# Kernel optimization log

Measured on AMD Instinct MI355X. Metric: run time of the kernel, lower is better.

Reference implementation:

```python
import jax, jax.numpy as jnp
import numpy as np

H = 16          # num_heads
EPS = 1e-6      # RMSNorm eps


def setup_inputs() -> dict:
    key = jax.random.key(0)
    ks = jax.random.split(key, 5)
    B, N, D = 4, 4096, 1024
    x = jax.random.normal(ks[0], (B, N, D), dtype=jnp.float32)
    q = jax.random.normal(ks[1], (D,), dtype=jnp.float32)
    k = jax.random.normal(ks[2], (D,), dtype=jnp.float32)
    log_decay = jax.random.normal(ks[3], (H,), dtype=jnp.float32)
    norm_weight = jnp.ones((D,), dtype=jnp.float32)
    o_w = jax.random.normal(ks[4], (D, D), dtype=jnp.float32) * 0.02
    return {"x": x, "q": q, "k": k, "log_decay": log_decay,
            "norm_weight": norm_weight, "o_w": o_w}


def reference(x, q, k, log_decay, norm_weight, o_w):
    b, n, dm = x.shape
    dh = dm // H
    qh = q.reshape(H, dh)            # per-head query vector (constant over b, n)
    kh = k.reshape(H, dh)            # per-head key vector
    v = x.reshape(b, n, H, dh)       # values = input tokens
    # exp(logsigmoid(a)) == sigmoid(a): per-head decay in (0, 1)
    lam = jax.nn.sigmoid(log_decay)  # (H,)

    def step(S, v_t):
        # S: (b, H, dh, dh) recurrent state;  v_t: (b, H, dh)
        S = lam[None, :, None, None] * S + kh[None, :, :, None] * v_t[:, :, None, :]
        o_t = jnp.einsum('hd,bhdv->bhv', qh, S)
        return S, o_t

    S0 = jnp.zeros((b, H, dh, dh), dtype=x.dtype)
    _, o = jax.lax.scan(step, S0, jnp.moveaxis(v, 1, 0))  # o: (n, b, H, dh)
    o = jnp.moveaxis(o, 0, 1).reshape(b, n, dm)

    # RMSNorm over the channel dim
    o = o * jax.lax.rsqrt(jnp.mean(o * o, axis=-1, keepdims=True) + EPS) * norm_weight
    # o_proj (no bias)
    return o @ o_w.T
```

## Files before the change

### kernel.cpp

```cpp
#include <hip/hip_runtime.h>
#include <hip/hip_bf16.h>
#include <cstdint>
#include <cstddef>

#define HH   16
#define BB   4
#define NN   4096
#define DD   1024
#define MM   (BB * NN)
#define NC   128
#define LC   32
#define EPSV 1e-6f

typedef short short8 __attribute__((ext_vector_type(8)));
typedef float floatx4 __attribute__((ext_vector_type(4)));

__device__ __forceinline__ void async_copy16(const void* g, void* l) {
    __builtin_amdgcn_global_load_lds(
        (const __attribute__((address_space(1))) void*)g,
        (__attribute__((address_space(3))) void*)l, 16, 0, 0);
}

__device__ __forceinline__ uint2 pack_bf16x4(float a, float b, float c, float d) {
    union { __hip_bfloat16 h[4]; uint2 u; } cv;
    cv.h[0] = __float2bfloat16(a); cv.h[1] = __float2bfloat16(b);
    cv.h[2] = __float2bfloat16(c); cv.h[3] = __float2bfloat16(d);
    return cv.u;
}

__global__ void k_meta(const float* __restrict__ q, const float* __restrict__ k,
                       const float* __restrict__ ld, float* __restrict__ meta) {
    int tid = threadIdx.x;
    float p = q[tid] * k[tid];
    #pragma unroll
    for (int off = 32; off > 0; off >>= 1) p += __shfl_xor(p, off);
    if ((tid & 63) == 0) meta[16 + (tid >> 6)] = p;
    if (tid < HH) meta[tid] = 1.f / (1.f + expf(-ld[tid]));
}

__global__ void k_wconv(const float* __restrict__ ow, const float* __restrict__ nw,
                        __hip_bfloat16* __restrict__ wp) {
    size_t i4 = (size_t)blockIdx.x * 256 + threadIdx.x;
    int j = (int)((i4 * 4) & (DD - 1));
    float4 v = ((const float4*)ow)[i4];
    ((uint2*)wp)[i4] = pack_bf16x4(v.x * nw[j], v.y * nw[j + 1],
                                   v.z * nw[j + 2], v.w * nw[j + 3]);
}

__global__ void k_chunk_end(const float* __restrict__ x, const float* __restrict__ meta,
                            float* __restrict__ E) {
    int b = blockIdx.x >> 7, c = blockIdx.x & (NC - 1);
    int j4 = threadIdx.x;
    float lam = meta[(j4 * 4) >> 6];
    const float4* xp = (const float4*)(x + ((size_t)(b * NN + c * LC)) * DD) + j4;
    float4 e = {0.f, 0.f, 0.f, 0.f};
    #pragma unroll
    for (int t = 0; t < LC; ++t) {
        float4 v = xp[(size_t)t * (DD / 4)];
        e.x = fmaf(lam, e.x, v.x); e.y = fmaf(lam, e.y, v.y);
        e.z = fmaf(lam, e.z, v.z); e.w = fmaf(lam, e.w, v.w);
    }
    ((float4*)(E + (size_t)blockIdx.x * DD))[j4] = e;
}

__global__ void k_carry(const float* __restrict__ meta, const float* __restrict__ E,
                        float* __restrict__ P) {
    __shared__ float tile[NC][33];
    int b = blockIdx.x >> 5, jg = blockIdx.x & 31;
    int tid = threadIdx.x;
    int cc = tid >> 5, jj = tid & 31;
    #pragma unroll
    for (int it = 0; it < 16; ++it) {
        int c = it * 8 + cc;
        tile[c][jj] = E[(size_t)(b * NC + c) * DD + jg * 32 + jj];
    }
    __syncthreads();
    if (tid < 32) {
        int j = jg * 32 + tid;
        float lam = meta[j >> 6];
        float lamL = lam;
        lamL *= lamL; lamL *= lamL; lamL *= lamL; lamL *= lamL; lamL *= lamL;
        float p = 0.f;
        for (int c = 0; c < NC; ++c) {
            float e = tile[c][tid];
            tile[c][tid] = p;
            p = fmaf(lamL, p, e);
        }
    }
    __syncthreads();
    #pragma unroll
    for (int it = 0; it < 16; ++it) {
        int c = it * 8 + cc;
        P[(size_t)(b * NC + c) * DD + jg * 32 + jj] = tile[c][jj];
    }
}

__global__ void k_scan(const float* __restrict__ x, const float* __restrict__ meta,
                       const float* __restrict__ P, __hip_bfloat16* __restrict__ obf,
                       float* __restrict__ sumsq) {
    __shared__ float ssq[4][LC];
    int b = blockIdx.x >> 7, c = blockIdx.x & (NC - 1);
    int j4 = threadIdx.x;
    int h = (j4 * 4) >> 6;
    float lam = meta[h];
    float ch  = meta[16 + h];
    int row0 = b * NN + c * LC;
    int lane = threadIdx.x & 63, w = threadIdx.x >> 6;
    const float4* xp = (const float4*)(x + (size_t)row0 * DD) + j4;
    float4 y = ((const float4*)(P + (size_t)blockIdx.x * DD))[j4];
    for (int t = 0; t < LC; ++t) {
        float4 v = xp[(size_t)t * (DD / 4)];
        y.x = fmaf(lam, y.x, v.x); y.y = fmaf(lam, y.y, v.y);
        y.z = fmaf(lam, y.z, v.z); y.w = fmaf(lam, y.w, v.w);
        float ox = ch * y.x, oy = ch * y.y, oz = ch * y.z, ow = ch * y.w;
        ((uint2*)(obf + (size_t)(row0 + t) * DD))[j4] = pack_bf16x4(ox, oy, oz, ow);
        float s = ox * ox + oy * oy + oz * oz + ow * ow;
        #pragma unroll
        for (int off = 32; off > 0; off >>= 1) s += __shfl_xor(s, off);
        if (lane == 0) ssq[w][t] = s;
    }
    __syncthreads();
    if (threadIdx.x < LC) {
        int t = threadIdx.x;
        sumsq[row0 + t] = ssq[0][t] + ssq[1][t] + ssq[2][t] + ssq[3][t];
    }
}

#define GEMM_STAGE(BUF, MAT, KK, TN)                                           \
  do {                                                                         \
    const short* _src = (MAT) ? Wg : Ag;                                       \
    const int _b0 = (MAT) ? n0 : m0;                                           \
    char* _dst = (char*)&lds[BUF][MAT][KK][0] + w * 1024;                      \
    _Pragma("unroll") for (int _i = 0; _i < 2; ++_i)                           \
      async_copy16(_src + (size_t)(_b0 + _i * 128 + rr) * 1024                 \
                        + (TN) * 64 + (KK) * 32 + oo * 8,                      \
                   _dst + _i * 8192);                                          \
  } while (0)

#define GEMM_REGION(BUF, KK)                                                   \
  do {                                                                         \
    short8 af[8]; short8 bf[4];                                                \
    _Pragma("unroll") for (int mt = 0; mt < 8; ++mt)                           \
      af[mt] = *(const short8*)(&lds[BUF][0][KK][0] +                          \
                                (arow_base + mt * 16) * 32 + p_rd * 8);        \
    _Pragma("unroll") for (int nt = 0; nt < 4; ++nt)                           \
      bf[nt] = *(const short8*)(&lds[BUF][1][KK][0] +                          \
                                (brow_base + nt * 16) * 32 + p_rd * 8);        \
    __builtin_amdgcn_s_setprio(1);                                             \
    _Pragma("unroll") for (int mt = 0; mt < 8; ++mt) {                         \
      _Pragma("unroll") for (int nt = 0; nt < 4; ++nt)                         \
        acc[mt][nt] = __builtin_amdgcn_mfma_f32_16x16x32_bf16(                 \
            af[mt], bf[nt], acc[mt][nt], 0, 0, 0);                             \
    }                                                                          \
    __builtin_amdgcn_s_setprio(0);                                             \
  } while (0)

__launch_bounds__(512, 2)
__global__ void k_gemm(const __hip_bfloat16* __restrict__ A,
                       const __hip_bfloat16* __restrict__ W,
                       const float* __restrict__ sumsq, float* __restrict__ out) {
    __shared__ __attribute__((aligned(16))) short lds[2][2][2][256 * 32];
    const int tid = threadIdx.x;
    const int lane = tid & 63, w = tid >> 6;
    const int wm = w >> 2, wn = w & 3;
    const int g = blockIdx.x;
    const int xcd = g & 7, idx = g >> 3;
    const int bm = xcd * 8 + (idx >> 2);
    const int bn = idx & 3;
    const int m0 = bm * 256, n0 = bn * 256;
    const short* Ag = (const short*)A;
    const short* Wg = (const short*)W;

    const int rr = tid >> 2;
    const int oo = (tid & 3) ^ ((rr >> 1) & 3);

    const int p_rd = (lane >> 4) ^ (((lane & 15) >> 1) & 3);
    const int arow_base = wm * 128 + (lane & 15);
    const int brow_base = wn * 64 + (lane & 15);

    floatx4 acc[8][4] = {};

    GEMM_STAGE(0, 0, 0, 0); GEMM_STAGE(0, 1, 0, 0);
    GEMM_STAGE(0, 0, 1, 0); GEMM_STAGE(0, 1, 1, 0);

    for (int t = 0; t < 16; ++t) {
        const int buf = t & 1;
        asm volatile("s_waitcnt vmcnt(4)" ::: "memory");
        __builtin_amdgcn_s_barrier();
        if (t < 15) { GEMM_STAGE(buf ^ 1, 0, 0, t + 1); GEMM_STAGE(buf ^ 1, 1, 0, t + 1); }
        GEMM_REGION(buf, 0);
        if (t < 15) {
            asm volatile("s_waitcnt vmcnt(4)" ::: "memory");
        } else {
            asm volatile("s_waitcnt vmcnt(0)" ::: "memory");
        }
        __builtin_amdgcn_s_barrier();
        if (t < 15) { GEMM_STAGE(buf ^ 1, 0, 1, t + 1); GEMM_STAGE(buf ^ 1, 1, 1, t + 1); }
        GEMM_REGION(buf, 1);
    }

    #pragma unroll
    for (int mt = 0; mt < 8; ++mt) {
        #pragma unroll
        for (int r = 0; r < 4; ++r) {
            int mrow = m0 + wm * 128 + mt * 16 + (lane >> 4) * 4 + r;
            float rs = rsqrtf(sumsq[mrow] * (1.f / 1024.f) + EPSV);
            #pragma unroll
            for (int nt = 0; nt < 4; ++nt) {
                int col = n0 + wn * 64 + nt * 16 + (lane & 15);
                out[(size_t)mrow * 1024 + col] = acc[mt][nt][r] * rs;
            }
        }
    }
}

extern "C" void kernel_launch(void* const* d_in, const int* in_sizes, int n_in,
                              void* d_out, int out_size, void* d_ws, size_t ws_size,
                              hipStream_t stream) {
    const float* x  = (const float*)d_in[0];
    const float* q  = (const float*)d_in[1];
    const float* k  = (const float*)d_in[2];
    const float* ld = (const float*)d_in[3];
    const float* nw = (const float*)d_in[4];
    const float* ow = (const float*)d_in[5];
    float* out = (float*)d_out;

    char* ws = (char*)d_ws;
    float* meta  = (float*)(ws + 0);
    float* sumsq = (float*)(ws + 256);
    float* E     = (float*)(ws + 65792);
    float* P     = (float*)(ws + 2162944);
    __hip_bfloat16* Wp  = (__hip_bfloat16*)(ws + 4260096);
    __hip_bfloat16* Obf = (__hip_bfloat16*)(ws + 6357248);

    k_meta<<<1, 1024, 0, stream>>>(q, k, ld, meta);
    k_wconv<<<(DD * DD / 4) / 256, 256, 0, stream>>>(ow, nw, Wp);
    k_chunk_end<<<BB * NC, 256, 0, stream>>>(x, meta, E);
    k_carry<<<BB * 32, 256, 0, stream>>>(meta, E, P);
    k_scan<<<BB * NC, 256, 0, stream>>>(x, meta, P, Obf, sumsq);
    k_gemm<<<(MM / 256) * (DD / 256), 512, 0, stream>>>(Obf, Wp, sumsq, out);
}
```

Before: 176.3 us.

## Inline meta computation into consumers and deepen GEMM pipeline to 4-stage ring

Removes the k_meta launch by computing sigmoid decay and the per-head q·k dot product inside the scan kernels (with a 16-lane shuffle reduction in k_scan). The GEMM main loop moves from double-buffered halves of a 64-wide K tile to a 4-slot ring of 32-wide K slices, with three slices prefetched ahead and one barrier per slice. The aim is to cut a kernel launch and hide more global-load latency in the GEMM. The cost is more barriers per K and some redundant sigmoid/dot work per block.

```diff
diff --git a/kernel.cpp b/kernel.cpp
--- a/kernel.cpp
+++ b/kernel.cpp
@@ -28,14 +28,8 @@
     return cv.u;
 }
 
-__global__ void k_meta(const float* __restrict__ q, const float* __restrict__ k,
-                       const float* __restrict__ ld, float* __restrict__ meta) {
-    int tid = threadIdx.x;
-    float p = q[tid] * k[tid];
-    #pragma unroll
-    for (int off = 32; off > 0; off >>= 1) p += __shfl_xor(p, off);
-    if ((tid & 63) == 0) meta[16 + (tid >> 6)] = p;
-    if (tid < HH) meta[tid] = 1.f / (1.f + expf(-ld[tid]));
+__device__ __forceinline__ float sigmoidf(float a) {
+    return 1.f / (1.f + expf(-a));
 }
 
 __global__ void k_wconv(const float* __restrict__ ow, const float* __restrict__ nw,
@@ -47,11 +41,11 @@
                                    v.z * nw[j + 2], v.w * nw[j + 3]);
 }
 
-__global__ void k_chunk_end(const float* __restrict__ x, const float* __restrict__ meta,
+__global__ void k_chunk_end(const float* __restrict__ x, const float* __restrict__ ld,
                             float* __restrict__ E) {
     int b = blockIdx.x >> 7, c = blockIdx.x & (NC - 1);
     int j4 = threadIdx.x;
-    float lam = meta[(j4 * 4) >> 6];
+    float lam = sigmoidf(ld[j4 >> 4]);
     const float4* xp = (const float4*)(x + ((size_t)(b * NN + c * LC)) * DD) + j4;
     float4 e = {0.f, 0.f, 0.f, 0.f};
     #pragma unroll
@@ -63,7 +57,7 @@
     ((float4*)(E + (size_t)blockIdx.x * DD))[j4] = e;
 }
 
-__global__ void k_carry(const float* __restrict__ meta, const float* __restrict__ E,
+__global__ void k_carry(const float* __restrict__ ld, const float* __restrict__ E,
                         float* __restrict__ P) {
     __shared__ float tile[NC][33];
     int b = blockIdx.x >> 5, jg = blockIdx.x & 31;
@@ -77,7 +71,7 @@
     __syncthreads();
     if (tid < 32) {
         int j = jg * 32 + tid;
-        float lam = meta[j >> 6];
+        float lam = sigmoidf(ld[j >> 6]);
         float lamL = lam;
         lamL *= lamL; lamL *= lamL; lamL *= lamL; lamL *= lamL; lamL *= lamL;
         float p = 0.f;
@@ -95,15 +89,20 @@
     }
 }
 
-__global__ void k_scan(const float* __restrict__ x, const float* __restrict__ meta,
+__global__ void k_scan(const float* __restrict__ x, const float* __restrict__ q,
+                       const float* __restrict__ k, const float* __restrict__ ld,
                        const float* __restrict__ P, __hip_bfloat16* __restrict__ obf,
                        float* __restrict__ sumsq) {
     __shared__ float ssq[4][LC];
     int b = blockIdx.x >> 7, c = blockIdx.x & (NC - 1);
     int j4 = threadIdx.x;
-    int h = (j4 * 4) >> 6;
-    float lam = meta[h];
-    float ch  = meta[16 + h];
+    int h = j4 >> 4;
+    float lam = sigmoidf(ld[h]);
+    float4 q4 = ((const float4*)q)[j4];
+    float4 k4 = ((const float4*)k)[j4];
+    float ch = q4.x * k4.x + q4.y * k4.y + q4.z * k4.z + q4.w * k4.w;
+    #pragma unroll
+    for (int off = 1; off < 16; off <<= 1) ch += __shfl_xor(ch, off);
     int row0 = b * NN + c * LC;
     int lane = threadIdx.x & 63, w = threadIdx.x >> 6;
     const float4* xp = (const float4*)(x + (size_t)row0 * DD) + j4;
@@ -126,26 +125,28 @@
     }
 }
 
-#define GEMM_STAGE(BUF, MAT, KK, TN)                                           \
+#define GEMM_STAGE(SLOT, S)                                                    \
   do {                                                                         \
-    const short* _src = (MAT) ? Wg : Ag;                                       \
-    const int _b0 = (MAT) ? n0 : m0;                                           \
-    char* _dst = (char*)&lds[BUF][MAT][KK][0] + w * 1024;                      \
+    char* _da = (char*)&lds[SLOT][0][0] + w * 1024;                            \
+    char* _db = (char*)&lds[SLOT][1][0] + w * 1024;                            \
     _Pragma("unroll") for (int _i = 0; _i < 2; ++_i)                           \
-      async_copy16(_src + (size_t)(_b0 + _i * 128 + rr) * 1024                 \
-                        + (TN) * 64 + (KK) * 32 + oo * 8,                      \
-                   _dst + _i * 8192);                                          \
+      async_copy16(Ag + (size_t)(m0 + _i * 128 + rr) * 1024 + (S) * 32 + oo * 8, \
+                   _da + _i * 8192);                                           \
+    _Pragma("unroll") for (int _i = 0; _i < 2; ++_i)                           \
+      async_copy16(Wg + (size_t)(n0 + _i * 128 + rr) * 1024 + (S) * 32 + oo * 8, \
+                   _db + _i * 8192);                                           \
   } while (0)
 
-#define GEMM_REGION(BUF, KK)                                                   \
+#define GEMM_CONSUME(SLOT)                                                     \
   do {                                                                         \
     short8 af[8]; short8 bf[4];                                                \
+    const short* _a = &lds[SLOT][0][0];                                        \
+    const short* _b = &lds[SLOT][1][0];                                        \
     _Pragma("unroll") for (int mt = 0; mt < 8; ++mt)                           \
-      af[mt] = *(const short8*)(&lds[BUF][0][KK][0] +                          \
-                                (arow_base + mt * 16) * 32 + p_rd * 8);        \
+      af[mt] = *(const short8*)(_a + (arow_base + mt * 16) * 32 + p_rd * 8);   \
     _Pragma("unroll") for (int nt = 0; nt < 4; ++nt)                           \
-      bf[nt] = *(const short8*)(&lds[BUF][1][KK][0] +                          \
-                                (brow_base + nt * 16) * 32 + p_rd * 8);        \
+      bf[nt] = *(const short8*)(_b + (brow_base + nt * 16) * 32 + p_rd * 8);   \
+    asm volatile("s_waitcnt lgkmcnt(0)" ::: "memory");                         \
     __builtin_amdgcn_s_setprio(1);                                             \
     _Pragma("unroll") for (int mt = 0; mt < 8; ++mt) {                         \
       _Pragma("unroll") for (int nt = 0; nt < 4; ++nt)                         \
@@ -159,7 +160,7 @@
 __global__ void k_gemm(const __hip_bfloat16* __restrict__ A,
                        const __hip_bfloat16* __restrict__ W,
                        const float* __restrict__ sumsq, float* __restrict__ out) {
-    __shared__ __attribute__((aligned(16))) short lds[2][2][2][256 * 32];
+    __shared__ __attribute__((aligned(16))) short lds[4][2][256 * 32];
     const int tid = threadIdx.x;
     const int lane = tid & 63, w = tid >> 6;
     const int wm = w >> 2, wn = w & 3;
@@ -180,24 +181,23 @@
 
     floatx4 acc[8][4] = {};
 
-    GEMM_STAGE(0, 0, 0, 0); GEMM_STAGE(0, 1, 0, 0);
-    GEMM_STAGE(0, 0, 1, 0); GEMM_STAGE(0, 1, 1, 0);
-
-    for (int t = 0; t < 16; ++t) {
-        const int buf = t & 1;
-        asm volatile("s_waitcnt vmcnt(4)" ::: "memory");
+    GEMM_STAGE(0, 0); GEMM_STAGE(1, 1); GEMM_STAGE(2, 2);
+
+    for (int s = 0; s < 29; ++s) {
+        asm volatile("s_waitcnt vmcnt(8)" ::: "memory");
         __builtin_amdgcn_s_barrier();
-        if (t < 15) { GEMM_STAGE(buf ^ 1, 0, 0, t + 1); GEMM_STAGE(buf ^ 1, 1, 0, t + 1); }
-        GEMM_REGION(buf, 0);
-        if (t < 15) {
-            asm volatile("s_waitcnt vmcnt(4)" ::: "memory");
-        } else {
-            asm volatile("s_waitcnt vmcnt(0)" ::: "memory");
-        }
-        __builtin_amdgcn_s_barrier();
-        if (t < 15) { GEMM_STAGE(buf ^ 1, 0, 1, t + 1); GEMM_STAGE(buf ^ 1, 1, 1, t + 1); }
-        GEMM_REGION(buf, 1);
-    }
+        GEMM_STAGE((s + 3) & 3, s + 3);
+        GEMM_CONSUME(s & 3);
+    }
+    asm volatile("s_waitcnt vmcnt(8)" ::: "memory");
+    __builtin_amdgcn_s_barrier();
+    GEMM_CONSUME(1);
+    asm volatile("s_waitcnt vmcnt(4)" ::: "memory");
+    __builtin_amdgcn_s_barrier();
+    GEMM_CONSUME(2);
+    asm volatile("s_waitcnt vmcnt(0)" ::: "memory");
+    __builtin_amdgcn_s_barrier();
+    GEMM_CONSUME(3);
 
     #pragma unroll
     for (int mt = 0; mt < 8; ++mt) {
@@ -226,17 +226,15 @@
     float* out = (float*)d_out;
 
     char* ws = (char*)d_ws;
-    float* meta  = (float*)(ws + 0);
     float* sumsq = (float*)(ws + 256);
     float* E     = (float*)(ws + 65792);
     float* P     = (float*)(ws + 2162944);
     __hip_bfloat16* Wp  = (__hip_bfloat16*)(ws + 4260096);
     __hip_bfloat16* Obf = (__hip_bfloat16*)(ws + 6357248);
 
-    k_meta<<<1, 1024, 0, stream>>>(q, k, ld, meta);
     k_wconv<<<(DD * DD / 4) / 256, 256, 0, stream>>>(ow, nw, Wp);
-    k_chunk_end<<<BB * NC, 256, 0, stream>>>(x, meta, E);
-    k_carry<<<BB * 32, 256, 0, stream>>>(meta, E, P);
-    k_scan<<<BB * NC, 256, 0, stream>>>(x, meta, P, Obf, sumsq);
+    k_chunk_end<<<BB * NC, 256, 0, stream>>>(x, ld, E);
+    k_carry<<<BB * 32, 256, 0, stream>>>(ld, E, P);
+    k_scan<<<BB * NC, 256, 0, stream>>>(x, q, k, ld, P, Obf, sumsq);
     k_gemm<<<(MM / 256) * (DD / 256), 512, 0, stream>>>(Obf, Wp, sumsq, out);
 }
```

Result: no change. 174.3 us (-1.2%).
